# Kernel optimization log

Measured on AMD Instinct MI355X. Metric: run time of the kernel, lower is better.

Reference implementation:

```python
import jax, jax.numpy as jnp
import numpy as np

NUM_EMBEDDINGS = 1024
EMBEDDING_DIM = 256
E_LOSS_WEIGHT = 0.25
MU = 0.01
EPSILON = 1e-05
N_TOKENS = 65536


def setup_inputs() -> dict:
    key = jax.random.key(0)
    k1, k2, k3 = jax.random.split(key, 3)
    return {
        "inputs": jax.random.normal(k1, (N_TOKENS, EMBEDDING_DIM), dtype=jnp.float32),
        "embedding_weight": jax.random.normal(k2, (NUM_EMBEDDINGS, EMBEDDING_DIM), dtype=jnp.float32),
        "ema_w": jax.random.normal(k3, (NUM_EMBEDDINGS, EMBEDDING_DIM), dtype=jnp.float32),
        "ema_cluster_size": jnp.zeros((NUM_EMBEDDINGS,), dtype=jnp.float32),
    }


def reference(inputs, embedding_weight, ema_w, ema_cluster_size):
    N, D = inputs.shape
    K = embedding_weight.shape[0]

    # Squared L2 distances: [N, K]
    distances = (
        jnp.sum(inputs ** 2, axis=1, keepdims=True)
        + jnp.sum(embedding_weight ** 2, axis=1)
        - 2.0 * (inputs @ embedding_weight.T)
    )
    idx = jnp.argmin(distances, axis=1)              # [N]

    # Gather codebook entries (replaces one-hot @ weight)
    quantized_raw = embedding_weight[idx]            # [N, D]

    # Commitment loss (quantized detached)
    e_latent_loss = jnp.mean((jax.lax.stop_gradient(quantized_raw) - inputs) ** 2)
    loss = E_LOSS_WEIGHT * e_latent_loss

    # Per-code counts and scatter-sum of inputs (replaces one-hot matmuls)
    counts = jax.ops.segment_sum(jnp.ones((N,), inputs.dtype), idx, num_segments=K)  # [K]
    dw = jax.ops.segment_sum(inputs, idx, num_segments=K)                             # [K, D]

    # EMA updates (training branch)
    new_cluster = ema_cluster_size * (1.0 - MU) + MU * counts
    n = jnp.sum(new_cluster)
    new_cluster = (new_cluster + EPSILON) / (n + K * EPSILON) * n
    new_ema_w = ema_w * (1.0 - MU) + MU * dw
    new_embedding = new_ema_w / new_cluster[:, None]

    # Straight-through estimator
    quantized = inputs + jax.lax.stop_gradient(quantized_raw - inputs)

    avg_probs = counts / N
    perplexity = jnp.exp(-jnp.sum(avg_probs * jnp.log(avg_probs + 1e-10)))

    encoding_indices = idx.reshape(N, 1)
    return quantized, loss, encoding_indices, perplexity, new_cluster, new_ema_w, new_embedding
```

## Files before the change

kernel.cpp:

```cpp
#include <hip/hip_runtime.h>

typedef _Float16 half8 __attribute__((ext_vector_type(8)));
typedef _Float16 half4 __attribute__((ext_vector_type(4)));
typedef float f32x4 __attribute__((ext_vector_type(4)));

#define N_TOK 65536
#define DIM   256
#define KCODE 1024
#define MU_C  0.01f
#define EPS_C 1e-5f

#define O_Q    0
#define O_LOSS 16777216
#define O_IDX  16777217
#define O_PERP 16842753
#define O_NC   16842754
#define O_NEW  16843778
#define O_EMB  17105922

#define W_IDX   0
#define W_CNT   65536
#define W_CUR   66560
#define W_OFF   67584
#define W_CNTF  68608
#define W_NFLAG 69632
#define W_ELAT  69633
#define W_FLAG  69696
#define W_ORDER 135232
#define W_DW    200768
#define W_WSQ   462912
#define W_WH    463936
#define W_XSQF  595008
#define W_ELATA 660544
#define W_PACK  676928

__device__ __forceinline__ int imin(int a, int b) { return a < b ? a : b; }
__device__ __forceinline__ int imax(int a, int b) { return a > b ? a : b; }

__global__ void convert_wsq(const float* __restrict__ W, _Float16* __restrict__ Wh,
                            float* __restrict__ wsq) {
    int gid = blockIdx.x * 256 + threadIdx.x;
    int row = gid >> 6, lane = gid & 63;
    float4 v = *(const float4*)(W + (size_t)row * 256 + lane * 4);
    half4 h;
    h[0] = (_Float16)v.x; h[1] = (_Float16)v.y; h[2] = (_Float16)v.z; h[3] = (_Float16)v.w;
    *(half4*)(Wh + (size_t)row * 256 + lane * 4) = h;
    float s = v.x * v.x + v.y * v.y + v.z * v.z + v.w * v.w;
#pragma unroll
    for (int off = 1; off < 64; off <<= 1) s += __shfl_xor(s, off);
    if (lane == 0) wsq[row] = s;
}

__global__ __launch_bounds__(256, 4) void argmin_mfma(
    const float* __restrict__ X, const _Float16* __restrict__ Wh,
    const float* __restrict__ wsq, int* __restrict__ idx_out,
    unsigned* __restrict__ nflag, int* __restrict__ flaglist)
{
    __shared__ _Float16 Bs[2][32 * 256];

    const int tid  = threadIdx.x;
    const int lane = tid & 63;
    const int w    = tid >> 6;
    const int l15  = lane & 15;
    const int lk   = lane >> 4;
    const int t0   = blockIdx.x * 64;

    half8 a[8];
    {
        const float* xr = X + (size_t)(t0 + w * 16 + l15) * 256 + lk * 8;
#pragma unroll
        for (int g = 0; g < 8; ++g) {
            float4 u0 = *(const float4*)(xr + g * 32);
            float4 u1 = *(const float4*)(xr + g * 32 + 4);
            half8 h;
            h[0] = (_Float16)u0.x; h[1] = (_Float16)u0.y;
            h[2] = (_Float16)u0.z; h[3] = (_Float16)u0.w;
            h[4] = (_Float16)u1.x; h[5] = (_Float16)u1.y;
            h[6] = (_Float16)u1.z; h[7] = (_Float16)u1.w;
            a[g] = h;
        }
    }

    int u1a[4], u2a[4];
#pragma unroll
    for (int i = 0; i < 4; ++i) { u1a[i] = 0x7FFFFFFF; u2a[i] = 0x7FFFFFFF; }

#define STAGE(cc, bb)                                                          \
    _Pragma("unroll")                                                          \
    for (int i = 0; i < 4; ++i) {                                              \
        int loff = (w * 4 + i) * 1024;                                         \
        int off  = loff + lane * 16;                                           \
        int row  = off >> 9;                                                   \
        int slot = (off >> 4) & 31;                                            \
        const _Float16* src = Wh + (size_t)((cc) * 32 + row) * 256             \
                                 + ((slot ^ (row & 7)) << 3);                  \
        __builtin_amdgcn_global_load_lds(                                      \
            (const __attribute__((address_space(1))) void*)src,                \
            (__attribute__((address_space(3))) void*)((char*)Bs[bb] + loff),   \
            16, 0, 0);                                                         \
    }

    STAGE(0, 0);
    __syncthreads();

    for (int c = 0; c < 32; ++c) {
        const int cur = c & 1;
        if (c < 31) { STAGE(c + 1, cur ^ 1); }

        f32x4 acc[2];
        acc[0] = (f32x4)0.0f; acc[1] = (f32x4)0.0f;

        __builtin_amdgcn_s_setprio(1);
#pragma unroll
        for (int ks = 0; ks < 4; ++ks) {
#pragma unroll
            for (int kk = 0; kk < 2; ++kk) {
                int slot = ks * 8 + kk * 4 + lk;
                int sw   = (slot ^ (l15 & 7)) << 4;
                half8 b0 = *(const half8*)((const char*)Bs[cur] + l15 * 512 + sw);
                half8 b1 = *(const half8*)((const char*)Bs[cur] + (16 + l15) * 512 + sw);
                acc[0] = __builtin_amdgcn_mfma_f32_16x16x32_f16(
                    a[ks * 2 + kk], b0, acc[0], 0, 0, 0);
                acc[1] = __builtin_amdgcn_mfma_f32_16x16x32_f16(
                    a[ks * 2 + kk], b1, acc[1], 0, 0, 0);
            }
        }
        __builtin_amdgcn_s_setprio(0);

#pragma unroll
        for (int nf = 0; nf < 2; ++nf) {
            int   code = c * 32 + nf * 16 + l15;
            float tc   = fmaf(0.5f, wsq[code], 512.0f);
#pragma unroll
            for (int r = 0; r < 4; ++r) {
                float sv = tc - acc[nf][r];
                int u = (__float_as_int(sv) & 0xFFFFFC00) | code;
                u2a[r] = imin(u2a[r], imax(u1a[r], u));
                u1a[r] = imin(u1a[r], u);
            }
        }
        __syncthreads();
    }
#undef STAGE

#pragma unroll
    for (int r = 0; r < 4; ++r) {
#pragma unroll
        for (int off = 1; off < 16; off <<= 1) {
            int b1 = __shfl_xor(u1a[r], off);
            int b2 = __shfl_xor(u2a[r], off);
            int n2 = imin(imin(u2a[r], b2), imax(u1a[r], b1));
            u1a[r] = imin(u1a[r], b1);
            u2a[r] = n2;
        }
    }
    if (l15 == 0) {
#pragma unroll
        for (int r = 0; r < 4; ++r) {
            int row = t0 + w * 16 + lk * 4 + r;
            idx_out[row] = u1a[r] & 1023;
            float s1 = __int_as_float(u1a[r] & 0xFFFFFC00);
            float s2 = __int_as_float(u2a[r] & 0xFFFFFC00);
            if (s2 - s1 < 0.125f) {
                unsigned p = atomicAdd(nflag, 1u);
                flaglist[p] = row;
            }
        }
    }
}

__global__ void cleanup_xsq(const float* __restrict__ X,
                            const unsigned* __restrict__ nflagp,
                            const int* __restrict__ flaglist,
                            float* __restrict__ xsqf) {
    int n = (int)nflagp[0];
    int wid  = (blockIdx.x * 256 + threadIdx.x) >> 6;
    int lane = threadIdx.x & 63;
    for (int i = wid; i < n; i += 1024) {
        const float* row = X + (size_t)flaglist[i] * 256;
        float4 v = *(const float4*)(row + lane * 4);
        float s = v.x * v.x + v.y * v.y + v.z * v.z + v.w * v.w;
#pragma unroll
        for (int off = 1; off < 64; off <<= 1) s += __shfl_xor(s, off);
        if (lane == 0) xsqf[i] = s;
    }
}

__global__ __launch_bounds__(256, 2) void cleanup_gemm(
    const float* __restrict__ X, const float* __restrict__ W,
    const float* __restrict__ wsq, const unsigned* __restrict__ nflagp,
    const int* __restrict__ flaglist, const float* __restrict__ xsqf,
    unsigned long long* __restrict__ pack)
{
    __shared__ float xs [16][64];
    __shared__ float wps[16][128];
    __shared__ float wsq_s[128];

    const int n = (int)nflagp[0];
    const int tid = threadIdx.x;
    const int tx  = tid & 15;
    const int ty  = tid >> 4;
    const int c0    = (blockIdx.x & 7) * 128;
    const int tslot = blockIdx.x >> 3;
    const int srow_x = tid & 63,  sq_x = tid >> 6;
    const int srow_w = tid & 127, sh_w = tid >> 7;

    if (tid < 128) wsq_s[tid] = wsq[c0 + tid];

    for (int tile = tslot; tile * 64 < n; tile += 256) {
        const int t0 = tile * 64;
        const int gtok = flaglist[imin(t0 + srow_x, n - 1)];
        const float* xrow = X + (size_t)gtok * DIM;
        const float* wrow = W + (size_t)(c0 + srow_w) * DIM + sh_w * 8;

        float xsq_r[4];
#pragma unroll
        for (int i = 0; i < 4; ++i) xsq_r[i] = xsqf[imin(t0 + ty * 4 + i, n - 1)];

        float minv[4]; int mini[4];
#pragma unroll
        for (int i = 0; i < 4; ++i) { minv[i] = 3.402823466e+38f; mini[i] = 0; }

        float acc[4][8];
#pragma unroll
        for (int i = 0; i < 4; ++i)
#pragma unroll
            for (int j = 0; j < 8; ++j) acc[i][j] = 0.0f;

        float4 xa = *(const float4*)(xrow + sq_x * 4);
        float4 wa = *(const float4*)(wrow);
        float4 wb = *(const float4*)(wrow + 4);

        for (int ks = 0; ks < 16; ++ks) {
            __syncthreads();
            xs[sq_x * 4 + 0][srow_x] = xa.x; xs[sq_x * 4 + 1][srow_x] = xa.y;
            xs[sq_x * 4 + 2][srow_x] = xa.z; xs[sq_x * 4 + 3][srow_x] = xa.w;
            wps[sh_w * 8 + 0][srow_w] = wa.x; wps[sh_w * 8 + 1][srow_w] = wa.y;
            wps[sh_w * 8 + 2][srow_w] = wa.z; wps[sh_w * 8 + 3][srow_w] = wa.w;
            wps[sh_w * 8 + 4][srow_w] = wb.x; wps[sh_w * 8 + 5][srow_w] = wb.y;
            wps[sh_w * 8 + 6][srow_w] = wb.z; wps[sh_w * 8 + 7][srow_w] = wb.w;
            __syncthreads();
            if (ks < 15) {
                xa = *(const float4*)(xrow + (ks + 1) * 16 + sq_x * 4);
                wa = *(const float4*)(wrow + (ks + 1) * 16);
                wb = *(const float4*)(wrow + (ks + 1) * 16 + 4);
            }
#pragma unroll
            for (int kl = 0; kl < 16; ++kl) {
                float4 av = *(const float4*)&xs [kl][ty * 4];
                float4 b0 = *(const float4*)&wps[kl][tx * 8];
                float4 b1 = *(const float4*)&wps[kl][tx * 8 + 4];
                float aa[4] = {av.x, av.y, av.z, av.w};
                float bb[8] = {b0.x, b0.y, b0.z, b0.w, b1.x, b1.y, b1.z, b1.w};
#pragma unroll
                for (int i = 0; i < 4; ++i)
#pragma unroll
                    for (int j = 0; j < 8; ++j)
                        acc[i][j] = fmaf(aa[i], bb[j], acc[i][j]);
            }
        }
#pragma unroll
        for (int i = 0; i < 4; ++i) {
#pragma unroll
            for (int j = 0; j < 8; ++j) {
                float t1 = xsq_r[i] + wsq_s[tx * 8 + j];
                float s  = t1 - 2.0f * acc[i][j];
                int   cc = c0 + tx * 8 + j;
                if (s < minv[i]) { minv[i] = s; mini[i] = cc; }
            }
        }
#pragma unroll
        for (int i = 0; i < 4; ++i) {
#pragma unroll
            for (int off = 1; off < 16; off <<= 1) {
                float ov = __shfl_xor(minv[i], off);
                int   oi = __shfl_xor(mini[i], off);
                if (ov < minv[i] || (ov == minv[i] && oi < mini[i])) {
                    minv[i] = ov; mini[i] = oi;
                }
            }
        }
        if (tx == 0) {
#pragma unroll
            for (int i = 0; i < 4; ++i) {
                int pos = t0 + ty * 4 + i;
                if (pos < n) {
                    unsigned long long pu =
                        ((unsigned long long)(unsigned)__float_as_int(minv[i]) << 32)
                        | (unsigned)mini[i];
                    atomicMin(&pack[pos], pu);
                }
            }
        }
        __syncthreads();
    }
}

__global__ void cleanup_write(const unsigned* __restrict__ nflagp,
                              const int* __restrict__ flaglist,
                              const unsigned long long* __restrict__ pack,
                              int* __restrict__ idx_out) {
    int n = (int)nflagp[0];
    for (int i = blockIdx.x * 256 + threadIdx.x; i < n; i += 65536)
        idx_out[flaglist[i]] = (int)(pack[i] & 0xFFFFFFFFull);
}

__global__ __launch_bounds__(256) void epilogue_token(
    const float* __restrict__ X, const float* __restrict__ W,
    const int* __restrict__ idx, float* __restrict__ out,
    float* __restrict__ elat_arr, unsigned* __restrict__ cnt)
{
    int gid = blockIdx.x * 256 + threadIdx.x;
    int t = gid >> 6, q = gid & 63;
    int code = idx[t];
    float4 x4 = ((const float4*)X)[gid];
    float4 w4 = ((const float4*)W)[(size_t)code * 64 + q];
    ((float4*)(out + O_Q))[gid] = w4;
    float dx0 = w4.x - x4.x, dx1 = w4.y - x4.y, dx2 = w4.z - x4.z, dx3 = w4.w - x4.w;
    float e = dx0 * dx0 + dx1 * dx1 + dx2 * dx2 + dx3 * dx3;
    if (q == 0) {
        out[O_IDX + t] = (float)code;
        atomicAdd(&cnt[code], 1u);
    }
#pragma unroll
    for (int off = 1; off < 64; off <<= 1) e += __shfl_xor(e, off);
    __shared__ float se[4];
    int lane = threadIdx.x & 63, wid = threadIdx.x >> 6;
    if (lane == 0) se[wid] = e;
    __syncthreads();
    if (threadIdx.x == 0) elat_arr[blockIdx.x] = se[0] + se[1] + se[2] + se[3];
}

__global__ __launch_bounds__(256) void k_scan(const unsigned* __restrict__ cnt,
                                              unsigned* __restrict__ offs,
                                              float* __restrict__ cntf) {
    int t = threadIdx.x, lane = t & 63, wid = t >> 6;
    uint4 v = ((const uint4*)cnt)[t];
    cntf[4 * t + 0] = (float)v.x; cntf[4 * t + 1] = (float)v.y;
    cntf[4 * t + 2] = (float)v.z; cntf[4 * t + 3] = (float)v.w;
    unsigned s = v.x + v.y + v.z + v.w;
    unsigned ps = s;
#pragma unroll
    for (int off = 1; off < 64; off <<= 1) {
        unsigned o = __shfl_up(ps, off);
        if (lane >= off) ps += o;
    }
    __shared__ unsigned wsum[4];
    if (lane == 63) wsum[wid] = ps;
    __syncthreads();
    unsigned base = 0;
#pragma unroll
    for (int i = 0; i < 4; ++i) if (i < wid) base += wsum[i];
    unsigned excl = base + ps - s;
    offs[4 * t + 0] = excl;
    offs[4 * t + 1] = excl + v.x;
    offs[4 * t + 2] = excl + v.x + v.y;
    offs[4 * t + 3] = excl + v.x + v.y + v.z;
}

__global__ void k_scatter(const int* __restrict__ idx, const unsigned* __restrict__ offs,
                          unsigned* __restrict__ cursor, int* __restrict__ order) {
    int t = blockIdx.x * 256 + threadIdx.x;
    int c = idx[t];
    unsigned p = atomicAdd(&cursor[c], 1u);
    order[offs[c] + p] = t;
}

__global__ __launch_bounds__(256) void k_dw(const float* __restrict__ X,
                                            const int* __restrict__ order,
                                            const int* __restrict__ idx,
                                            float* __restrict__ dw)
{
    int gw   = (blockIdx.x * 256 + threadIdx.x) >> 6;
    int lane = threadIdx.x & 63;
    int p0 = gw * 16;
    float4 acc = make_float4(0.f, 0.f, 0.f, 0.f);
    int cur = -1;
#pragma unroll 4
    for (int i = 0; i < 16; ++i) {
        int t = order[p0 + i];
        int c = idx[t];
        float4 x4 = *(const float4*)(X + (size_t)t * 256 + lane * 4);
        if (c != cur) {
            if (cur >= 0) {
                float* dwp = dw + (size_t)cur * 256 + lane * 4;
                atomicAdd(dwp + 0, acc.x); atomicAdd(dwp + 1, acc.y);
                atomicAdd(dwp + 2, acc.z); atomicAdd(dwp + 3, acc.w);
            }
            cur = c; acc = x4;
        } else {
            acc.x += x4.x; acc.y += x4.y; acc.z += x4.z; acc.w += x4.w;
        }
    }
    if (cur >= 0) {
        float* dwp = dw + (size_t)cur * 256 + lane * 4;
        atomicAdd(dwp + 0, acc.x); atomicAdd(dwp + 1, acc.y);
        atomicAdd(dwp + 2, acc.z); atomicAdd(dwp + 3, acc.w);
    }
}

__global__ __launch_bounds__(1024) void finalize_small(
    const float* __restrict__ ecs, const float* __restrict__ counts,
    const float* __restrict__ elat_arr, float* __restrict__ out)
{
    int k = threadIdx.x;
    float cnt = counts[k];
    float nc = ecs[k] * (1.0f - MU_C) + MU_C * cnt;
    float p = cnt * (1.0f / 65536.0f);
    float h = p * logf(p + 1e-10f);
    float el = 0.f;
#pragma unroll
    for (int i = 0; i < 16; ++i) el += elat_arr[k + i * 1024];
    float rn = nc, rh = h, re = el;
#pragma unroll
    for (int off = 1; off < 64; off <<= 1) {
        rn += __shfl_xor(rn, off);
        rh += __shfl_xor(rh, off);
        re += __shfl_xor(re, off);
    }
    __shared__ float sn[16], sh[16], sef[16];
    int wid = k >> 6, lane = k & 63;
    if (lane == 0) { sn[wid] = rn; sh[wid] = rh; sef[wid] = re; }
    __syncthreads();
    float n = 0.0f, H = 0.0f, E = 0.0f;
#pragma unroll
    for (int i = 0; i < 16; ++i) { n += sn[i]; H += sh[i]; E += sef[i]; }
    out[O_NC + k] = (nc + EPS_C) / (n + 1024.0f * EPS_C) * n;
    if (k == 0) {
        out[O_LOSS] = 0.25f * (E * (1.0f / 16777216.0f));
        out[O_PERP] = expf(-H);
    }
}

__global__ void finalize_embed(const float* __restrict__ ema_w,
                               const float* __restrict__ dw, float* __restrict__ out)
{
    int gid = blockIdx.x * blockDim.x + threadIdx.x;
    int k = gid >> 8;
    float ew = ema_w[gid] * (1.0f - MU_C) + MU_C * dw[gid];
    out[O_NEW + gid] = ew;
    out[O_EMB + gid] = ew / out[O_NC + k];
}

extern "C" void kernel_launch(void* const* d_in, const int* in_sizes, int n_in,
                              void* d_out, int out_size, void* d_ws, size_t ws_size,
                              hipStream_t stream) {
    const float* X     = (const float*)d_in[0];
    const float* W     = (const float*)d_in[1];
    const float* ema_w = (const float*)d_in[2];
    const float* ecs   = (const float*)d_in[3];
    float*    out    = (float*)d_out;
    unsigned* wsu    = (unsigned*)d_ws;
    float*    wsf    = (float*)d_ws;
    int*      idx    = (int*)d_ws + W_IDX;
    unsigned* cnt    = wsu + W_CNT;
    unsigned* cursor = wsu + W_CUR;
    unsigned* offs   = wsu + W_OFF;
    float*    cntf   = wsf + W_CNTF;
    unsigned* nflag  = wsu + W_NFLAG;
    int*      flags  = (int*)d_ws + W_FLAG;
    int*      order  = (int*)d_ws + W_ORDER;
    float*    dw     = wsf + W_DW;
    float*    wsq    = wsf + W_WSQ;
    _Float16* Wh     = (_Float16*)(wsu + W_WH);
    float*    xsqf   = wsf + W_XSQF;
    float*    elatA  = wsf + W_ELATA;
    unsigned long long* pack = (unsigned long long*)(wsu + W_PACK);

    hipMemsetAsync(wsu + W_CNT, 0, 4098 * sizeof(unsigned), stream);
    hipMemsetAsync(wsf + W_DW,  0, 262144 * sizeof(float),  stream);
    hipMemsetAsync(pack, 0xFF, 65536 * sizeof(unsigned long long), stream);
    hipLaunchKernelGGL(convert_wsq,    dim3(256),   dim3(256),  0, stream, W, Wh, wsq);
    hipLaunchKernelGGL(argmin_mfma,    dim3(1024),  dim3(256),  0, stream, X, Wh, wsq, idx, nflag, flags);
    hipLaunchKernelGGL(cleanup_xsq,    dim3(256),   dim3(256),  0, stream, X, nflag, flags, xsqf);
    hipLaunchKernelGGL(cleanup_gemm,   dim3(2048),  dim3(256),  0, stream, X, W, wsq, nflag, flags, xsqf, pack);
    hipLaunchKernelGGL(cleanup_write,  dim3(256),   dim3(256),  0, stream, nflag, flags, pack, idx);
    hipLaunchKernelGGL(epilogue_token, dim3(16384), dim3(256),  0, stream, X, W, idx, out, elatA, cnt);
    hipLaunchKernelGGL(k_scan,         dim3(1),     dim3(256),  0, stream, cnt, offs, cntf);
    hipLaunchKernelGGL(k_scatter,      dim3(256),   dim3(256),  0, stream, idx, offs, cursor, order);
    hipLaunchKernelGGL(k_dw,           dim3(1024),  dim3(256),  0, stream, X, order, idx, dw);
    hipLaunchKernelGGL(finalize_small, dim3(1),     dim3(1024), 0, stream, ecs, cntf, elatA, out);
    hipLaunchKernelGGL(finalize_embed, dim3(1024),  dim3(256),  0, stream, ema_w, dw, out);
}
```

Before: 233.7 us.

## Retile argmin GEMM to 256 tokens per block, split codebook halves

The argmin kernel now gives each wave 64 tokens instead of 16, so every B fragment read from LDS feeds four MFMAs. The codebook is split into two halves across blocks so the grid stays at 512 blocks. A new merge kernel combines the per-half top-two results and builds the ambiguity flag list, and it reuses the dw buffer as scratch, so the dw memset moves after the merge. This trades higher register use (launch bounds drop to 2 blocks per unit) and an extra small kernel for less LDS traffic and fewer redundant weight loads per token.

```diff
diff --git a/kernel.cpp b/kernel.cpp
--- a/kernel.cpp
+++ b/kernel.cpp
@@ -51,10 +51,9 @@
     if (lane == 0) wsq[row] = s;
 }
 
-__global__ __launch_bounds__(256, 4) void argmin_mfma(
+__global__ __launch_bounds__(256, 2) void argmin_mfma(
     const float* __restrict__ X, const _Float16* __restrict__ Wh,
-    const float* __restrict__ wsq, int* __restrict__ idx_out,
-    unsigned* __restrict__ nflag, int* __restrict__ flaglist)
+    const float* __restrict__ wsq, unsigned long long* __restrict__ halfres)
 {
     __shared__ _Float16 Bs[2][32 * 256];
 
@@ -63,11 +62,14 @@
     const int w    = tid >> 6;
     const int l15  = lane & 15;
     const int lk   = lane >> 4;
-    const int t0   = blockIdx.x * 64;
-
-    half8 a[8];
-    {
-        const float* xr = X + (size_t)(t0 + w * 16 + l15) * 256 + lk * 8;
+    const int half  = blockIdx.x & 1;
+    const int cbase = half * 512;
+    const int t0    = (blockIdx.x >> 1) * 256;
+
+    half8 a[4][8];
+#pragma unroll
+    for (int g2 = 0; g2 < 4; ++g2) {
+        const float* xr = X + (size_t)(t0 + w * 64 + g2 * 16 + l15) * 256 + lk * 8;
 #pragma unroll
         for (int g = 0; g < 8; ++g) {
             float4 u0 = *(const float4*)(xr + g * 32);
@@ -77,13 +79,13 @@
             h[2] = (_Float16)u0.z; h[3] = (_Float16)u0.w;
             h[4] = (_Float16)u1.x; h[5] = (_Float16)u1.y;
             h[6] = (_Float16)u1.z; h[7] = (_Float16)u1.w;
-            a[g] = h;
-        }
-    }
-
-    int u1a[4], u2a[4];
-#pragma unroll
-    for (int i = 0; i < 4; ++i) { u1a[i] = 0x7FFFFFFF; u2a[i] = 0x7FFFFFFF; }
+            a[g2][g] = h;
+        }
+    }
+
+    int u1a[16], u2a[16];
+#pragma unroll
+    for (int i = 0; i < 16; ++i) { u1a[i] = 0x7FFFFFFF; u2a[i] = 0x7FFFFFFF; }
 
 #define STAGE(cc, bb)                                                          \
     _Pragma("unroll")                                                          \
@@ -92,8 +94,8 @@
         int off  = loff + lane * 16;                                           \
         int row  = off >> 9;                                                   \
         int slot = (off >> 4) & 31;                                            \
-        const _Float16* src = Wh + (size_t)((cc) * 32 + row) * 256             \
-                                 + ((slot ^ (row & 7)) << 3);                  \
+        const _Float16* src = Wh + (size_t)(cbase + (cc) * 32 + row) * 256     \
+                                 + ((slot ^ row) << 3);                        \
         __builtin_amdgcn_global_load_lds(                                      \
             (const __attribute__((address_space(1))) void*)src,                \
             (__attribute__((address_space(3))) void*)((char*)Bs[bb] + loff),   \
@@ -103,69 +105,87 @@
     STAGE(0, 0);
     __syncthreads();
 
-    for (int c = 0; c < 32; ++c) {
+    for (int c = 0; c < 16; ++c) {
         const int cur = c & 1;
-        if (c < 31) { STAGE(c + 1, cur ^ 1); }
-
-        f32x4 acc[2];
-        acc[0] = (f32x4)0.0f; acc[1] = (f32x4)0.0f;
+        if (c < 15) { STAGE(c + 1, cur ^ 1); }
+
+        f32x4 acc[4][2];
+#pragma unroll
+        for (int g2 = 0; g2 < 4; ++g2) { acc[g2][0] = (f32x4)0.0f; acc[g2][1] = (f32x4)0.0f; }
 
         __builtin_amdgcn_s_setprio(1);
 #pragma unroll
-        for (int ks = 0; ks < 4; ++ks) {
-#pragma unroll
-            for (int kk = 0; kk < 2; ++kk) {
-                int slot = ks * 8 + kk * 4 + lk;
-                int sw   = (slot ^ (l15 & 7)) << 4;
-                half8 b0 = *(const half8*)((const char*)Bs[cur] + l15 * 512 + sw);
-                half8 b1 = *(const half8*)((const char*)Bs[cur] + (16 + l15) * 512 + sw);
-                acc[0] = __builtin_amdgcn_mfma_f32_16x16x32_f16(
-                    a[ks * 2 + kk], b0, acc[0], 0, 0, 0);
-                acc[1] = __builtin_amdgcn_mfma_f32_16x16x32_f16(
-                    a[ks * 2 + kk], b1, acc[1], 0, 0, 0);
+        for (int ks = 0; ks < 8; ++ks) {
+            const int j = ks * 4 + lk;
+            const char* base = (const char*)Bs[cur];
+            half8 b0 = *(const half8*)(base + l15 * 512        + ((j ^ l15) << 4));
+            half8 b1 = *(const half8*)(base + (16 + l15) * 512 + ((j ^ (16 + l15)) << 4));
+#pragma unroll
+            for (int g2 = 0; g2 < 4; ++g2) {
+                acc[g2][0] = __builtin_amdgcn_mfma_f32_16x16x32_f16(
+                    a[g2][ks], b0, acc[g2][0], 0, 0, 0);
+                acc[g2][1] = __builtin_amdgcn_mfma_f32_16x16x32_f16(
+                    a[g2][ks], b1, acc[g2][1], 0, 0, 0);
             }
         }
         __builtin_amdgcn_s_setprio(0);
 
 #pragma unroll
         for (int nf = 0; nf < 2; ++nf) {
-            int   code = c * 32 + nf * 16 + l15;
+            int   code = cbase + c * 32 + nf * 16 + l15;
             float tc   = fmaf(0.5f, wsq[code], 512.0f);
 #pragma unroll
-            for (int r = 0; r < 4; ++r) {
-                float sv = tc - acc[nf][r];
-                int u = (__float_as_int(sv) & 0xFFFFFC00) | code;
-                u2a[r] = imin(u2a[r], imax(u1a[r], u));
-                u1a[r] = imin(u1a[r], u);
-            }
+            for (int g2 = 0; g2 < 4; ++g2)
+#pragma unroll
+                for (int r = 0; r < 4; ++r) {
+                    float sv = tc - acc[g2][nf][r];
+                    int u = (__float_as_int(sv) & 0xFFFFFC00) | code;
+                    int s = g2 * 4 + r;
+                    u2a[s] = imin(u2a[s], imax(u1a[s], u));
+                    u1a[s] = imin(u1a[s], u);
+                }
         }
         __syncthreads();
     }
 #undef STAGE
 
 #pragma unroll
-    for (int r = 0; r < 4; ++r) {
+    for (int s = 0; s < 16; ++s) {
 #pragma unroll
         for (int off = 1; off < 16; off <<= 1) {
-            int b1 = __shfl_xor(u1a[r], off);
-            int b2 = __shfl_xor(u2a[r], off);
-            int n2 = imin(imin(u2a[r], b2), imax(u1a[r], b1));
-            u1a[r] = imin(u1a[r], b1);
-            u2a[r] = n2;
+            int b1 = __shfl_xor(u1a[s], off);
+            int b2 = __shfl_xor(u2a[s], off);
+            int n2 = imin(imin(u2a[s], b2), imax(u1a[s], b1));
+            u1a[s] = imin(u1a[s], b1);
+            u2a[s] = n2;
         }
     }
     if (l15 == 0) {
 #pragma unroll
-        for (int r = 0; r < 4; ++r) {
-            int row = t0 + w * 16 + lk * 4 + r;
-            idx_out[row] = u1a[r] & 1023;
-            float s1 = __int_as_float(u1a[r] & 0xFFFFFC00);
-            float s2 = __int_as_float(u2a[r] & 0xFFFFFC00);
-            if (s2 - s1 < 0.125f) {
-                unsigned p = atomicAdd(nflag, 1u);
-                flaglist[p] = row;
-            }
-        }
+        for (int s = 0; s < 16; ++s) {
+            int row = t0 + w * 64 + (s >> 2) * 16 + lk * 4 + (s & 3);
+            halfres[(size_t)half * 65536 + row] =
+                ((unsigned long long)(unsigned)u1a[s] << 32) | (unsigned)u2a[s];
+        }
+    }
+}
+
+__global__ void merge_halves(const unsigned long long* __restrict__ halfres,
+                             int* __restrict__ idx_out,
+                             unsigned* __restrict__ nflag, int* __restrict__ flaglist)
+{
+    int t = blockIdx.x * 256 + threadIdx.x;
+    unsigned long long A = halfres[t], B = halfres[65536 + t];
+    int a1 = (int)(A >> 32), a2 = (int)(unsigned)A;
+    int b1 = (int)(B >> 32), b2 = (int)(unsigned)B;
+    int u1 = imin(a1, b1);
+    int u2 = imin(imax(a1, b1), imin(a2, b2));
+    idx_out[t] = u1 & 1023;
+    float s1 = __int_as_float(u1 & 0xFFFFFC00);
+    float s2 = __int_as_float(u2 & 0xFFFFFC00);
+    if (s2 - s1 < 0.125f) {
+        unsigned p = atomicAdd(nflag, 1u);
+        flaglist[p] = t;
     }
 }
 
@@ -465,13 +485,15 @@
     _Float16* Wh     = (_Float16*)(wsu + W_WH);
     float*    xsqf   = wsf + W_XSQF;
     float*    elatA  = wsf + W_ELATA;
-    unsigned long long* pack = (unsigned long long*)(wsu + W_PACK);
+    unsigned long long* pack    = (unsigned long long*)(wsu + W_PACK);
+    unsigned long long* halfres = (unsigned long long*)(wsf + W_DW);
 
     hipMemsetAsync(wsu + W_CNT, 0, 4098 * sizeof(unsigned), stream);
-    hipMemsetAsync(wsf + W_DW,  0, 262144 * sizeof(float),  stream);
     hipMemsetAsync(pack, 0xFF, 65536 * sizeof(unsigned long long), stream);
     hipLaunchKernelGGL(convert_wsq,    dim3(256),   dim3(256),  0, stream, W, Wh, wsq);
-    hipLaunchKernelGGL(argmin_mfma,    dim3(1024),  dim3(256),  0, stream, X, Wh, wsq, idx, nflag, flags);
+    hipLaunchKernelGGL(argmin_mfma,    dim3(512),   dim3(256),  0, stream, X, Wh, wsq, halfres);
+    hipLaunchKernelGGL(merge_halves,   dim3(256),   dim3(256),  0, stream, halfres, idx, nflag, flags);
+    hipMemsetAsync(wsf + W_DW, 0, 262144 * sizeof(float), stream);
     hipLaunchKernelGGL(cleanup_xsq,    dim3(256),   dim3(256),  0, stream, X, nflag, flags, xsqf);
     hipLaunchKernelGGL(cleanup_gemm,   dim3(2048),  dim3(256),  0, stream, X, W, wsq, nflag, flags, xsqf, pack);
     hipLaunchKernelGGL(cleanup_write,  dim3(256),   dim3(256),  0, stream, nflag, flags, pack, idx);
```

Result: slower. 240.3 us (+2.8%).
